# Optimization experiments

Hardware: AMD Instinct MI355X
Metric: run time of the kernel (lower is better)

The kernel has to match this reference:

```python
import jax, jax.numpy as jnp
import numpy as np

DT = 0.002  # hardcoded dt0 in SDE.__call__
B, T, D = 4096, 2500, 3


def setup_inputs() -> dict:
    key = jax.random.key(0)
    ks = jax.random.split(key, 6)
    # drift/diffusion scaled by 0.1 so 2500-step Euler paths stay numerically stable in fp32
    return {
        "x0": jax.random.normal(ks[0], (B, D), jnp.float32),
        "drift": jax.random.normal(ks[1], (D, D), jnp.float32) * 0.1,
        "drift_bias": jax.random.normal(ks[2], (D,), jnp.float32),
        "diffusion": jax.random.normal(ks[3], (D, D), jnp.float32) * 0.1,
        "diffusion_bias": jax.random.normal(ks[4], (D,), jnp.float32) * 0.1,
        # standard-normal Brownian increments (scaled by sqrt(dt) inside reference)
        "noise": jax.random.normal(ks[5], (T, B, D), jnp.float32),
    }


def reference(x0, drift, drift_bias, diffusion, diffusion_bias, noise):
    # Euler-Maruyama: x_{k+1} = x_k + (A x_k + b) dt + diag(C x_k + d) dW_k
    # (diag(v) @ dW == v * dW elementwise), vmapped over batch via broadcasting.
    dt = jnp.asarray(DT, x0.dtype)
    sqrt_dt = jnp.sqrt(dt)

    def step(x, eps):
        dW = sqrt_dt * eps                       # [B, D]
        x_new = x + (x @ drift.T + drift_bias) * dt \
                + (x @ diffusion.T + diffusion_bias) * dW
        return x_new, x_new

    _, ys = jax.lax.scan(step, x0, noise)        # ys: [T, B, D]
    paths = jnp.concatenate([x0[None], ys], axis=0)  # [T+1, B, D], SaveAt includes t0
    return jnp.transpose(paths, (1, 0, 2))       # [B, T+1, D] like vmapped sol.ys
```

## Files before the change

### kernel.cpp

```cpp
#include <hip/hip_runtime.h>
#include <math.h>
#include <type_traits>


constexpr int B_N  = 4096;
constexpr int T_N  = 2500;
constexpr int CL   = 48;
constexpr int NFC  = T_N / CL;
constexpr int NCH  = NFC + 1;
constexpr int FLP  = 12;
constexpr int ROWF = (T_N + 1) * 3;

template <int N> using ic = std::integral_constant<int, N>;
typedef float f4v __attribute__((ext_vector_type(4)));


__global__ __launch_bounds__(64)
void sde_chunk_transforms(const float* __restrict__ A,
                          const float* __restrict__ bv,
                          const float* __restrict__ C,
                          const float* __restrict__ dv,
                          const float* __restrict__ noise,
                          float* __restrict__ trans)
{
    const int b = blockIdx.x * 64 + threadIdx.x;
    const int c = blockIdx.y;

    const float dt  = 0.002f;
    const float sdt = sqrtf(dt);

    float IA[3][3], Cs[3][3], bdt[3], ds[3];
#pragma unroll
    for (int i = 0; i < 3; ++i) {
        bdt[i] = bv[i] * dt;
        ds[i]  = dv[i] * sdt;
#pragma unroll
        for (int j = 0; j < 3; ++j) {
            IA[i][j] = A[i * 3 + j] * dt + (i == j ? 1.0f : 0.0f);
            Cs[i][j] = C[i * 3 + j] * sdt;
        }
    }

    float M[3][3] = {{1,0,0},{0,1,0},{0,0,1}};
    float v[3] = {0, 0, 0};

    const float* __restrict__ nb = noise + (size_t)c * CL * (B_N * 3) + (size_t)b * 3;
    const size_t nstride = (size_t)B_N * 3;

    float bufA[FLP][3], bufB[FLP][3];

    auto loadChunk = [&](float (&buf)[FLP][3], int s) {
#pragma unroll
        for (int k = 0; k < FLP; ++k) {
            const float* p = nb + ((size_t)s * FLP + k) * nstride;
            buf[k][0] = p[0];
            buf[k][1] = p[1];
            buf[k][2] = p[2];
        }
    };

    auto compChunk = [&](const float (&buf)[FLP][3]) {
#pragma unroll
        for (int k = 0; k < FLP; ++k) {
            const float e[3] = { buf[k][0], buf[k][1], buf[k][2] };
            float S[3][3], t[3];
#pragma unroll
            for (int i = 0; i < 3; ++i) {
                t[i] = fmaf(e[i], ds[i], bdt[i]);
#pragma unroll
                for (int j = 0; j < 3; ++j)
                    S[i][j] = fmaf(e[i], Cs[i][j], IA[i][j]);
            }
            float nM[3][3], nv[3];
#pragma unroll
            for (int i = 0; i < 3; ++i) {
#pragma unroll
                for (int j = 0; j < 3; ++j)
                    nM[i][j] = fmaf(S[i][2], M[2][j], fmaf(S[i][1], M[1][j], S[i][0] * M[0][j]));
                nv[i] = fmaf(S[i][2], v[2], fmaf(S[i][1], v[1], S[i][0] * v[0])) + t[i];
            }
#pragma unroll
            for (int i = 0; i < 3; ++i) {
                v[i] = nv[i];
#pragma unroll
                for (int j = 0; j < 3; ++j) M[i][j] = nM[i][j];
            }
        }
    };

    loadChunk(bufA, 0);
    loadChunk(bufB, 1);
    compChunk(bufA);
    loadChunk(bufA, 2);
    compChunk(bufB);
    loadChunk(bufB, 3);
    compChunk(bufA);
    compChunk(bufB);

    float* tp = trans + ((size_t)c * B_N + b) * 12;
    float4 w0 = { M[0][0], M[0][1], M[0][2], M[1][0] };
    float4 w1 = { M[1][1], M[1][2], M[2][0], M[2][1] };
    float4 w2 = { M[2][2], v[0],    v[1],    v[2]    };
    ((float4*)tp)[0] = w0;
    ((float4*)tp)[1] = w1;
    ((float4*)tp)[2] = w2;
}

__global__ __launch_bounds__(64)
void sde_scan(const float* __restrict__ x0,
              float* __restrict__ trans)
{
    const int b = blockIdx.x * 64 + threadIdx.x;

    float x[3] = { x0[b * 3 + 0], x0[b * 3 + 1], x0[b * 3 + 2] };

    float4* tp0 = (float4*)(trans + (size_t)b * 12);
    const size_t cs = (size_t)B_N * 3;

    float4 qa0, qa1, qa2, qb0, qb1, qb2, qc0, qc1, qc2, qd0, qd1, qd2;

    auto L = [&](int s, float4& r0, float4& r1, float4& r2) {
        const float4* tn = tp0 + (size_t)s * cs;
        r0 = tn[0]; r1 = tn[1]; r2 = tn[2];
    };
    auto useSlot = [&](int s, const float4& a0, const float4& a1, const float4& a2) {
        tp0[(size_t)s * cs] = make_float4(x[0], x[1], x[2], 0.0f);
        const float n0 = fmaf(a0.x, x[0], fmaf(a0.y, x[1], fmaf(a0.z, x[2], a2.y)));
        const float n1 = fmaf(a0.w, x[0], fmaf(a1.x, x[1], fmaf(a1.y, x[2], a2.z)));
        const float n2 = fmaf(a1.z, x[0], fmaf(a1.w, x[1], fmaf(a2.x, x[2], a2.w)));
        x[0] = n0; x[1] = n1; x[2] = n2;
    };

    L(0, qa0, qa1, qa2);
    L(1, qb0, qb1, qb2);
    L(2, qc0, qc1, qc2);
    L(3, qd0, qd1, qd2);

    for (int it = 0; it < NFC / 4; ++it) {
        const int s = it * 4;
        useSlot(s + 0, qa0, qa1, qa2);
        if (s + 4 < NFC) L(s + 4, qa0, qa1, qa2);
        useSlot(s + 1, qb0, qb1, qb2);
        if (s + 5 < NFC) L(s + 5, qb0, qb1, qb2);
        useSlot(s + 2, qc0, qc1, qc2);
        if (s + 6 < NFC) L(s + 6, qc0, qc1, qc2);
        useSlot(s + 3, qd0, qd1, qd2);
        if (s + 7 < NFC) L(s + 7, qd0, qd1, qd2);
    }

    tp0[(size_t)NFC * cs] = make_float4(x[0], x[1], x[2], 0.0f);
}

__global__ __launch_bounds__(64)
void sde_replay(const float* __restrict__ A,
                const float* __restrict__ bv,
                const float* __restrict__ C,
                const float* __restrict__ dv,
                const float* __restrict__ noise,
                const float* __restrict__ trans,
                float* __restrict__ out)
{
    __shared__ float tile[96][66];

    const int lane = threadIdx.x & 63;
    const int pg   = blockIdx.x & 63;
    const int c    = blockIdx.x >> 6;
    const int b    = (pg << 6) | lane;
    const int phi  = (11 * lane) & 15;

    const float dt  = 0.002f;
    const float sdt = sqrtf(dt);

    float Adt[3][3], Cs[3][3], bdt[3], dsv[3];
#pragma unroll
    for (int i = 0; i < 3; ++i) {
        bdt[i] = bv[i] * dt;
        dsv[i] = dv[i] * sdt;
#pragma unroll
        for (int j = 0; j < 3; ++j) {
            Adt[i][j] = A[i * 3 + j] * dt;
            Cs[i][j]  = C[i * 3 + j] * sdt;
        }
    }

    const f4v xb = __builtin_nontemporal_load(
        (const f4v*)(trans + ((size_t)c * B_N + b) * 12));
    float x0r = xb.x, x1r = xb.y, x2r = xb.z;

    const float* __restrict__ nb0 = noise + (size_t)b * 3;
    const size_t nstride = (size_t)B_N * 3;
    const int base48 = c * CL;

    auto stepf = [&](float e0, float e1, float e2) {
        const float a0 = fmaf(Adt[0][2], x2r, fmaf(Adt[0][1], x1r, fmaf(Adt[0][0], x0r, bdt[0])));
        const float a1 = fmaf(Adt[1][2], x2r, fmaf(Adt[1][1], x1r, fmaf(Adt[1][0], x0r, bdt[1])));
        const float a2 = fmaf(Adt[2][2], x2r, fmaf(Adt[2][1], x1r, fmaf(Adt[2][0], x0r, bdt[2])));

        const float c0 = fmaf(Cs[0][2], x2r, fmaf(Cs[0][1], x1r, fmaf(Cs[0][0], x0r, dsv[0])));
        const float c1 = fmaf(Cs[1][2], x2r, fmaf(Cs[1][1], x1r, fmaf(Cs[1][0], x0r, dsv[1])));
        const float c2 = fmaf(Cs[2][2], x2r, fmaf(Cs[2][1], x1r, fmaf(Cs[2][0], x0r, dsv[2])));

        x0r = fmaf(c0, e0, x0r + a0);
        x1r = fmaf(c1, e1, x1r + a1);
        x2r = fmaf(c2, e2, x2r + a2);
    };

    if (c == NFC) {
        float* op = out + (size_t)b * ROWF;
        if (phi == 0) {
            op[2496 * 3 + 0] = x0r; op[2496 * 3 + 1] = x1r; op[2496 * 3 + 2] = x2r;
        }
#pragma unroll
        for (int k = 0; k < 4; ++k) {
            const float* p = nb0 + (size_t)(2496 + k) * nstride;
            stepf(p[0], p[1], p[2]);
            const int j = k + 1;
            if (j >= phi) {
                float* d = op + (size_t)(2496 + j) * 3;
                d[0] = x0r; d[1] = x1r; d[2] = x2r;
            }
        }
        return;
    }

    const bool c0   = (c == 0);
    const bool last = (c == NFC - 1);

    auto tileWrite = [&](int j) {
        const int r = (j & 31) * 3;
        tile[r + 0][lane] = x0r;
        tile[r + 1][lane] = x1r;
        tile[r + 2][lane] = x2r;
    };

    auto rawGuard = [&]() {
        asm volatile("s_waitcnt lgkmcnt(0)" ::: "memory");
        __builtin_amdgcn_sched_barrier(0);
    };
    auto warGuard = [&]() {
        asm volatile("s_waitcnt lgkmcnt(0)" ::: "memory");
        __builtin_amdgcn_sched_barrier(0);
    };

    const int h   = lane >> 4;
    const int m   = lane & 15;
    const int phh = (11 * h) & 15;
    float* const outG = out + (size_t)(pg << 6) * ROWF + (size_t)base48 * 3;

    auto flush = [&](auto fc, bool maskTail) {
        constexpr int F = decltype(fc)::value;
        rawGuard();
#pragma unroll
        for (int i = 0; i < 16; ++i) {
            const int P    = 4 * i + h;
            const int phiP = (12 * i + phh) & 15;
            const int j    = phiP + 16 * F + m;
            const int r    = (j & 31) * 3;
            const float v0 = tile[r + 0][P];
            const float v1 = tile[r + 1][P];
            const float v2 = tile[r + 2][P];
            if (!maskTail || (phiP + m) <= 20) {
                float* d = outG + (size_t)P * ROWF + (size_t)j * 3;
                __builtin_nontemporal_store(v0, d + 0);
                __builtin_nontemporal_store(v1, d + 1);
                __builtin_nontemporal_store(v2, d + 2);
            }
        }
    };

    float bufA[16][3], bufB[16][3];
    auto loadN = [&](float (&buf)[16][3], int kbase, auto cnt) {
        constexpr int CNT = decltype(cnt)::value;
#pragma unroll
        for (int k = 0; k < CNT; ++k) {
            int g = base48 + kbase + k;
            g = g > (T_N - 1) ? (T_N - 1) : g;
            const float* p = nb0 + (size_t)g * nstride;
            buf[k][0] = p[0];
            buf[k][1] = p[1];
            buf[k][2] = p[2];
        }
    };

    loadN(bufA, 0,  ic<16>{});
    loadN(bufB, 16, ic<16>{});

    tileWrite(0);
    if (c0 && phi > 0) {
        float* d = outG + (size_t)lane * ROWF;
        d[0] = x0r; d[1] = x1r; d[2] = x2r;
    }

#pragma unroll
    for (int k = 0; k < 16; ++k) {
        stepf(bufA[k][0], bufA[k][1], bufA[k][2]);
        tileWrite(k + 1);
        if (c0 && (k + 1) < phi) {
            float* d = outG + (size_t)lane * ROWF + (size_t)(k + 1) * 3;
            d[0] = x0r; d[1] = x1r; d[2] = x2r;
        }
    }
    loadN(bufA, 32, ic<16>{});

#pragma unroll
    for (int k = 0; k < 15; ++k) {
        stepf(bufB[k][0], bufB[k][1], bufB[k][2]);
        tileWrite(k + 17);
    }
    loadN(bufB, 48, ic<14>{});

    flush(ic<0>{}, false);

    warGuard();
    stepf(bufB[15][0], bufB[15][1], bufB[15][2]);
    tileWrite(32);
#pragma unroll
    for (int k = 0; k < 15; ++k) {
        stepf(bufA[k][0], bufA[k][1], bufA[k][2]);
        tileWrite(33 + k);
    }

    flush(ic<1>{}, false);

    warGuard();
    stepf(bufA[15][0], bufA[15][1], bufA[15][2]);
    tileWrite(48);
#pragma unroll
    for (int k = 0; k < 14; ++k) {
        stepf(bufB[k][0], bufB[k][1], bufB[k][2]);
        tileWrite(49 + k);
    }

    flush(ic<2>{}, last);
}

extern "C" void kernel_launch(void* const* d_in, const int* in_sizes, int n_in,
                              void* d_out, int out_size, void* d_ws, size_t ws_size,
                              hipStream_t stream) {
    const float* x0    = (const float*)d_in[0];
    const float* A     = (const float*)d_in[1];
    const float* bv    = (const float*)d_in[2];
    const float* C     = (const float*)d_in[3];
    const float* dv    = (const float*)d_in[4];
    const float* noise = (const float*)d_in[5];
    float* out = (float*)d_out;

    float* trans = (float*)d_ws;

    dim3 gridPC(B_N / 64, NFC);

    sde_chunk_transforms<<<gridPC, 64, 0, stream>>>(A, bv, C, dv, noise, trans);
    sde_scan<<<B_N / 64, 64, 0, stream>>>(x0, trans);
    sde_replay<<<64 * NCH, 64, 0, stream>>>(A, bv, C, dv, noise, trans, out);
}
```

Before: 81.16 us.

## Enlarge time chunks to 64 steps and reverse replay block order

```diff
diff --git a/kernel.cpp b/kernel.cpp
--- a/kernel.cpp
+++ b/kernel.cpp
@@ -5,10 +5,10 @@
 
 constexpr int B_N  = 4096;
 constexpr int T_N  = 2500;
-constexpr int CL   = 48;
+constexpr int CL   = 64;
 constexpr int NFC  = T_N / CL;
 constexpr int NCH  = NFC + 1;
-constexpr int FLP  = 12;
+constexpr int FLP  = 8;
 constexpr int ROWF = (T_N + 1) * 3;
 
 template <int N> using ic = std::integral_constant<int, N>;
@@ -90,10 +90,12 @@
 
     loadChunk(bufA, 0);
     loadChunk(bufB, 1);
-    compChunk(bufA);
-    loadChunk(bufA, 2);
-    compChunk(bufB);
-    loadChunk(bufB, 3);
+    compChunk(bufA); loadChunk(bufA, 2);
+    compChunk(bufB); loadChunk(bufB, 3);
+    compChunk(bufA); loadChunk(bufA, 4);
+    compChunk(bufB); loadChunk(bufB, 5);
+    compChunk(bufA); loadChunk(bufA, 6);
+    compChunk(bufB); loadChunk(bufB, 7);
     compChunk(bufA);
     compChunk(bufB);
 
@@ -136,7 +138,7 @@
     L(2, qc0, qc1, qc2);
     L(3, qd0, qd1, qd2);
 
-    for (int it = 0; it < NFC / 4; ++it) {
+    for (int it = 0; it < 9; ++it) {
         const int s = it * 4;
         useSlot(s + 0, qa0, qa1, qa2);
         if (s + 4 < NFC) L(s + 4, qa0, qa1, qa2);
@@ -147,6 +149,9 @@
         useSlot(s + 3, qd0, qd1, qd2);
         if (s + 7 < NFC) L(s + 7, qd0, qd1, qd2);
     }
+    useSlot(36, qa0, qa1, qa2);
+    useSlot(37, qb0, qb1, qb2);
+    useSlot(38, qc0, qc1, qc2);
 
     tp0[(size_t)NFC * cs] = make_float4(x[0], x[1], x[2], 0.0f);
 }
@@ -164,7 +169,7 @@
 
     const int lane = threadIdx.x & 63;
     const int pg   = blockIdx.x & 63;
-    const int c    = blockIdx.x >> 6;
+    const int c    = (NCH - 1) - (blockIdx.x >> 6);
     const int b    = (pg << 6) | lane;
     const int phi  = (11 * lane) & 15;
 
@@ -189,7 +194,7 @@
 
     const float* __restrict__ nb0 = noise + (size_t)b * 3;
     const size_t nstride = (size_t)B_N * 3;
-    const int base48 = c * CL;
+    const int base = c * CL;
 
     auto stepf = [&](float e0, float e1, float e2) {
         const float a0 = fmaf(Adt[0][2], x2r, fmaf(Adt[0][1], x1r, fmaf(Adt[0][0], x0r, bdt[0])));
@@ -245,7 +250,7 @@
     const int h   = lane >> 4;
     const int m   = lane & 15;
     const int phh = (11 * h) & 15;
-    float* const outG = out + (size_t)(pg << 6) * ROWF + (size_t)base48 * 3;
+    float* const outG = out + (size_t)(pg << 6) * ROWF + (size_t)base * 3;
 
     auto flush = [&](auto fc, bool maskTail) {
         constexpr int F = decltype(fc)::value;
@@ -273,7 +278,7 @@
         constexpr int CNT = decltype(cnt)::value;
 #pragma unroll
         for (int k = 0; k < CNT; ++k) {
-            int g = base48 + kbase + k;
+            int g = base + kbase + k;
             g = g > (T_N - 1) ? (T_N - 1) : g;
             const float* p = nb0 + (size_t)g * nstride;
             buf[k][0] = p[0];
@@ -307,13 +312,13 @@
         stepf(bufB[k][0], bufB[k][1], bufB[k][2]);
         tileWrite(k + 17);
     }
-    loadN(bufB, 48, ic<14>{});
 
     flush(ic<0>{}, false);
 
     warGuard();
     stepf(bufB[15][0], bufB[15][1], bufB[15][2]);
     tileWrite(32);
+    loadN(bufB, 48, ic<16>{});
 #pragma unroll
     for (int k = 0; k < 15; ++k) {
         stepf(bufA[k][0], bufA[k][1], bufA[k][2]);
@@ -325,13 +330,25 @@
     warGuard();
     stepf(bufA[15][0], bufA[15][1], bufA[15][2]);
     tileWrite(48);
-#pragma unroll
-    for (int k = 0; k < 14; ++k) {
+    loadN(bufA, 64, ic<15>{});
+#pragma unroll
+    for (int k = 0; k < 15; ++k) {
         stepf(bufB[k][0], bufB[k][1], bufB[k][2]);
         tileWrite(49 + k);
     }
 
-    flush(ic<2>{}, last);
+    flush(ic<2>{}, false);
+
+    warGuard();
+    stepf(bufB[15][0], bufB[15][1], bufB[15][2]);
+    tileWrite(64);
+#pragma unroll
+    for (int k = 0; k < 15; ++k) {
+        stepf(bufA[k][0], bufA[k][1], bufA[k][2]);
+        tileWrite(65 + k);
+    }
+
+    flush(ic<3>{}, last);
 }
 
 extern "C" void kernel_launch(void* const* d_in, const int* in_sizes, int n_in,
```

Result: no change. 80.81 us, median of 2 (-0.4%).
